# Optimization experiments

Hardware: AMD Instinct MI355X
Metric: run time of the kernel (lower is better)

The kernel has to match this reference:

```python
import jax, jax.numpy as jnp
import numpy as np

B, S, D = 4, 1024, 1024
H, DK = 16, 64
E, DFF, TOPK = 8, 2048, 2
EPS = 1e-5

def setup_inputs() -> dict:
    key = jax.random.key(0)
    ks = jax.random.split(key, 8)
    sd = 0.02
    return {
        "x": jax.random.normal(ks[0], (B, S, D), jnp.float32),
        "Wqkv": jax.random.normal(ks[1], (3 * D, D), jnp.float32) * sd,
        "Wo": jax.random.normal(ks[2], (D, D), jnp.float32) * sd,
        "ln1_g": jnp.ones((D,), jnp.float32),
        "ln1_b": jnp.zeros((D,), jnp.float32),
        "ln2_g": jnp.ones((D,), jnp.float32),
        "ln2_b": jnp.zeros((D,), jnp.float32),
        "Wg": jax.random.normal(ks[3], (E, D), jnp.float32) * sd,
        "W1": jax.random.normal(ks[4], (E, DFF, D), jnp.float32) * sd,
        "W2": jax.random.normal(ks[5], (E, D, DFF), jnp.float32) * sd,
        "res_scale": jnp.ones((1,), jnp.float32),
    }

def _layernorm(x, g, b):
    mu = jnp.mean(x, axis=-1, keepdims=True)
    var = jnp.var(x, axis=-1, keepdims=True)
    return (x - mu) * jax.lax.rsqrt(var + EPS) * g + b

def _mha(x, Wqkv, Wo):
    # fused qkv projection (self-attention branch of original)
    qkv = jnp.einsum('bsd,ed->bse', x, Wqkv)  # [B,S,3D]
    q, k, v = jnp.split(qkv, 3, axis=-1)
    def heads(t):
        return t.reshape(B, S, H, DK).transpose(0, 2, 1, 3)  # [B,H,S,DK]
    q, k, v = heads(q), heads(k), heads(v)
    scores = jnp.einsum('bhqd,bhkd->bhqk', q, k) * (1.0 / np.sqrt(DK))
    attn = jax.nn.softmax(scores, axis=-1)
    ctx = jnp.einsum('bhqk,bhkd->bhqd', attn, v)
    ctx = ctx.transpose(0, 2, 1, 3).reshape(B, S, D)
    return jnp.einsum('bsd,od->bso', ctx, Wo)

def _moe(x, Wg, W1, W2):
    T = B * S
    flat = x.reshape(T, D)
    logits = flat @ Wg.T                      # [T,E]
    probs = jax.nn.softmax(logits, axis=-1)
    rw, sel = jax.lax.top_k(probs, TOPK)      # [T,K]
    rw = rw / jnp.sum(rw, axis=-1, keepdims=True)
    # dense all-experts FFN (faithful to original parallel_apply over all experts)
    h = jax.nn.gelu(jnp.einsum('td,efd->tef', flat, W1), approximate=False)  # [T,E,DFF]
    eo = jnp.einsum('tef,edf->ted', h, W2)    # [T,E,D]
    ew = jnp.zeros((T, E), flat.dtype).at[jnp.arange(T)[:, None], sel].add(rw)
    out = jnp.einsum('te,ted->td', ew, eo).reshape(B, S, D)
    logp = jnp.log(jnp.clip(probs, 1e-6))
    entropy_loss = jnp.mean(-jnp.sum(probs * logp, axis=-1))
    return out, logits, entropy_loss

def reference(x, Wqkv, Wo, ln1_g, ln1_b, ln2_g, ln2_b, Wg, W1, W2, res_scale):
    nx = _layernorm(x, ln1_g, ln1_b)
    x = x + _mha(nx, Wqkv, Wo) * res_scale
    nx = _layernorm(x, ln2_g, ln2_b)
    moe_out, router_logits, entropy_loss = _moe(nx, Wg, W1, W2)
    x = x + moe_out * res_scale
    return x, router_logits, entropy_loss
```

## Files before the change

### kernel.cpp

```cpp
#include <hip/hip_runtime.h>
#include <math.h>


typedef _Float16 f16;
typedef _Float16 f16x8 __attribute__((ext_vector_type(8)));
typedef _Float16 f16x4 __attribute__((ext_vector_type(4)));
typedef float f32x4 __attribute__((ext_vector_type(4)));

#define LO_SCALE 2048.0f
#define INV_LO   (1.0f/2048.0f)
#define INV_W    (1.0f/256.0f)
#define INV_WLO  (1.0f/(256.0f*2048.0f))

#define MFMA16(a, b, c) __builtin_amdgcn_mfma_f32_16x16x32_f16(a, b, c, 0, 0, 0)

__device__ __forceinline__ void gl_lds16(const void* g, void* l) {
  __builtin_amdgcn_global_load_lds(
      (const __attribute__((address_space(1))) void*)g,
      (__attribute__((address_space(3))) void*)l, 16, 0, 0);
}

__global__ __launch_bounds__(256) void cvt_w_kernel(
    const float* __restrict__ in, f16* __restrict__ oh, f16* __restrict__ ol, int n4) {
  const int i = blockIdx.x * 256 + threadIdx.x;
  if (i >= n4) return;
  const float4 v = ((const float4*)in)[i];
  f16x4 hv, lv;
  float a;
  a = v.x * 256.0f; hv[0] = (f16)a; lv[0] = (f16)((a - (float)hv[0]) * LO_SCALE);
  a = v.y * 256.0f; hv[1] = (f16)a; lv[1] = (f16)((a - (float)hv[1]) * LO_SCALE);
  a = v.z * 256.0f; hv[2] = (f16)a; lv[2] = (f16)((a - (float)hv[2]) * LO_SCALE);
  a = v.w * 256.0f; hv[3] = (f16)a; lv[3] = (f16)((a - (float)hv[3]) * LO_SCALE);
  ((f16x4*)oh)[i] = hv;
  ((f16x4*)ol)[i] = lv;
}

__global__ __launch_bounds__(256) void cvt_h_kernel(
    const float* __restrict__ in, f16* __restrict__ out, int n4) {
  const int i = blockIdx.x * 256 + threadIdx.x;
  if (i >= n4) return;
  const float4 v = ((const float4*)in)[i];
  f16x4 ov = {(f16)v.x, (f16)v.y, (f16)v.z, (f16)v.w};
  ((f16x4*)out)[i] = ov;
}

__global__ __launch_bounds__(256) void ln_kernel(
    const float* __restrict__ x, const float* __restrict__ g, const float* __restrict__ bb,
    f16* __restrict__ oh, f16* __restrict__ ol,
    f16* __restrict__ o1,
    float* __restrict__ of)
{
  const int t = blockIdx.x, tid = threadIdx.x;
  const float4 v = ((const float4*)(x + (long)t * 1024))[tid];
  float s  = v.x + v.y + v.z + v.w;
  float sq = v.x*v.x + v.y*v.y + v.z*v.z + v.w*v.w;
#pragma unroll
  for (int m = 1; m < 64; m <<= 1) { s += __shfl_xor(s, m); sq += __shfl_xor(sq, m); }
  __shared__ float red[8];
  const int w = tid >> 6;
  if ((tid & 63) == 0) { red[w] = s; red[4 + w] = sq; }
  __syncthreads();
  s  = red[0] + red[1] + red[2] + red[3];
  sq = red[4] + red[5] + red[6] + red[7];
  const float mu   = s * (1.0f/1024.0f);
  const float var  = sq * (1.0f/1024.0f) - mu*mu;
  const float rstd = 1.0f / sqrtf(var + 1e-5f);
  const float4 gv = ((const float4*)g)[tid];
  const float4 bv = ((const float4*)bb)[tid];
  float o4[4];
  o4[0] = (v.x - mu)*rstd*gv.x + bv.x;
  o4[1] = (v.y - mu)*rstd*gv.y + bv.y;
  o4[2] = (v.z - mu)*rstd*gv.z + bv.z;
  o4[3] = (v.w - mu)*rstd*gv.w + bv.w;
  const long base = (long)t * 1024 + tid * 4;
  if (oh) {
    f16x4 hv, lv;
#pragma unroll
    for (int i = 0; i < 4; ++i) {
      hv[i] = (f16)o4[i];
      lv[i] = (f16)((o4[i] - (float)hv[i]) * LO_SCALE);
    }
    *(f16x4*)(oh + base) = hv;
    *(f16x4*)(ol + base) = lv;
  }
  if (o1) {
    f16x4 ov = {(f16)o4[0], (f16)o4[1], (f16)o4[2], (f16)o4[3]};
    *(f16x4*)(o1 + base) = ov;
  }
  if (of) *(float4*)(of + base) = make_float4(o4[0], o4[1], o4[2], o4[3]);
}

#define GM_QKV 0
#define GM_WO  1

template<int MODE>
__global__ __launch_bounds__(256, 2) void gemm_split_kernel(
    const f16* __restrict__ Ah, const f16* __restrict__ Al,
    const f16* __restrict__ Bh, const f16* __restrict__ Bl,
    f16* __restrict__ Ch, f16* __restrict__ Cl,
    float* __restrict__ Cf,
    const float* __restrict__ xres, const float* __restrict__ rsp,
    int N, int K)
{
  __shared__ __align__(16) f16 sAh[128*32], sAl[128*32], sBh[128*32], sBl[128*32];
  const int tid = threadIdx.x;
  const int l = tid & 63, w = tid >> 6;
  const int wm = w >> 1, wn = w & 1;
  const int tm0 = blockIdx.y * 128, tn0 = blockIdx.x * 128;
  const int kg = l >> 4, r16 = l & 15;
  const int srow = w * 32 + (l >> 2);
  const int scol = (l & 3) * 8;
  const int ldsbase = w * 1024;

  f32x4 am[4][4] = {};
  f32x4 ac[4][4] = {};

  for (int k0 = 0; k0 < K; k0 += 32) {
#pragma unroll
    for (int i = 0; i < 2; ++i) {
      const int row = srow + i * 16;
      const long aoff = (long)(tm0 + row) * K + k0 + scol;
      const long boff = (long)(tn0 + row) * K + k0 + scol;
      const int lo = ldsbase + i * 512;
      gl_lds16(Ah + aoff, &sAh[lo]);
      gl_lds16(Al + aoff, &sAl[lo]);
      gl_lds16(Bh + boff, &sBh[lo]);
      gl_lds16(Bl + boff, &sBl[lo]);
    }
    __syncthreads();
    f16x8 ah[4], al[4], bh[4], bl[4];
#pragma unroll
    for (int m = 0; m < 4; ++m) {
      const int ro = (wm*64 + m*16 + r16) * 32 + kg*8;
      ah[m] = *(const f16x8*)&sAh[ro];
      al[m] = *(const f16x8*)&sAl[ro];
    }
#pragma unroll
    for (int n = 0; n < 4; ++n) {
      const int ro = (wn*64 + n*16 + r16) * 32 + kg*8;
      bh[n] = *(const f16x8*)&sBh[ro];
      bl[n] = *(const f16x8*)&sBl[ro];
    }
#pragma unroll
    for (int m = 0; m < 4; ++m)
#pragma unroll
      for (int n = 0; n < 4; ++n) {
        am[m][n] = MFMA16(ah[m], bh[n], am[m][n]);
        ac[m][n] = MFMA16(ah[m], bl[n], ac[m][n]);
        ac[m][n] = MFMA16(al[m], bh[n], ac[m][n]);
      }
    __syncthreads();
  }

  const float rs = (MODE == GM_WO) ? rsp[0] : 0.0f;
#pragma unroll
  for (int m = 0; m < 4; ++m)
#pragma unroll
    for (int n = 0; n < 4; ++n)
#pragma unroll
      for (int r = 0; r < 4; ++r) {
        const int row = tm0 + wm*64 + m*16 + kg*4 + r;
        const int col = tn0 + wn*64 + n*16 + r16;
        const long idx = (long)row * N + col;
        const float v = am[m][n][r] * INV_W + ac[m][n][r] * INV_WLO;
        if (MODE == GM_QKV) {
          const f16 vh = (f16)v;
          Ch[idx] = vh;
          Cl[idx] = (f16)((v - (float)vh) * LO_SCALE);
        } else {
          Cf[idx] = xres[idx] + rs * v;
        }
      }
}

__global__ __launch_bounds__(256, 2) void attn_kernel(
    const f16* __restrict__ qkh, const f16* __restrict__ qkl,
    f16* __restrict__ ctxh, f16* __restrict__ ctxl)
{
  __shared__ __align__(16) f16 sKh[64*64], sKl[64*64], sVh[64*64], sVl[64*64];
  __shared__ __align__(16) f16 sPh[4*16*64], sPl[4*16*64];
  const int qt = blockIdx.x;
  const int bh = blockIdx.y;
  const int b = bh >> 4, h = bh & 15;
  const int tid = threadIdx.x;
  const int l = tid & 63, w = tid >> 6;
  const int kg = l >> 4, r16 = l & 15;

  const long qbase = (long)(b*1024 + qt*64 + w*16 + r16) * 3072 + h * 64;
  f16x8 aqh[2], aql[2];
#pragma unroll
  for (int c = 0; c < 2; ++c) {
    aqh[c] = *(const f16x8*)(qkh + qbase + c*32 + kg*8);
    aql[c] = *(const f16x8*)(qkl + qbase + c*32 + kg*8);
  }

  f32x4 om[4] = {}; f32x4 oc[4] = {};
  float mrun[4] = {-INFINITY, -INFINITY, -INFINITY, -INFINITY};
  float lrun[4] = {0.f, 0.f, 0.f, 0.f};

  for (int kv0 = 0; kv0 < 1024; kv0 += 64) {
#pragma unroll
    for (int cc = 0; cc < 2; ++cc) {
      const int c = tid + cc * 256;
      const int row = c >> 3, c8 = c & 7;
      const long gb = (long)(b*1024 + kv0 + row) * 3072 + 1024 + h*64 + c8*8;
      const int slot = row*8 + (c8 ^ (row & 7));
      *(uint4*)&sKh[slot*8] = *(const uint4*)(qkh + gb);
      *(uint4*)&sKl[slot*8] = *(const uint4*)(qkl + gb);
      f16 vh8[8], vl8[8];
      *(uint4*)vh8 = *(const uint4*)(qkh + gb + 1024);
      *(uint4*)vl8 = *(const uint4*)(qkl + gb + 1024);
#pragma unroll
      for (int e2 = 0; e2 < 8; ++e2) {
        const int d = c8*8 + e2;
        const int ci = d*64 + (row ^ ((d & 7) << 3));
        sVh[ci] = vh8[e2];
        sVl[ci] = vl8[e2];
      }
    }
    __syncthreads();

    f32x4 sm[4] = {}; f32x4 sc[4] = {};
#pragma unroll
    for (int n = 0; n < 4; ++n) {
      const int krow = n*16 + r16;
#pragma unroll
      for (int c = 0; c < 2; ++c) {
        const int slot = krow*8 + ((c*4 + kg) ^ (krow & 7));
        const f16x8 kh = *(const f16x8*)&sKh[slot*8];
        const f16x8 kl = *(const f16x8*)&sKl[slot*8];
        sm[n] = MFMA16(aqh[c], kh, sm[n]);
        sc[n] = MFMA16(aqh[c], kl, sc[n]);
        sc[n] = MFMA16(aql[c], kh, sc[n]);
      }
    }
    float sval[4][4];
#pragma unroll
    for (int n = 0; n < 4; ++n)
#pragma unroll
      for (int r = 0; r < 4; ++r)
        sval[n][r] = (sm[n][r] + sc[n][r] * INV_LO) * 0.125f;

    float pv[4][4];
#pragma unroll
    for (int r = 0; r < 4; ++r) {
      float mx = fmaxf(fmaxf(sval[0][r], sval[1][r]), fmaxf(sval[2][r], sval[3][r]));
#pragma unroll
      for (int msk = 1; msk < 16; msk <<= 1) mx = fmaxf(mx, __shfl_xor(mx, msk));
      const float mnew = fmaxf(mrun[r], mx);
      const float fsc = expf(mrun[r] - mnew);
      mrun[r] = mnew;
      lrun[r] *= fsc;
#pragma unroll
      for (int n = 0; n < 4; ++n) { om[n][r] *= fsc; oc[n][r] *= fsc; }
      float ps = 0.f;
#pragma unroll
      for (int n = 0; n < 4; ++n) {
        const float p = expf(sval[n][r] - mnew);
        pv[n][r] = p;
        ps += p;
      }
#pragma unroll
      for (int msk = 1; msk < 16; msk <<= 1) ps += __shfl_xor(ps, msk);
      lrun[r] += ps;
    }

#pragma unroll
    for (int n = 0; n < 4; ++n)
#pragma unroll
      for (int r = 0; r < 4; ++r) {
        const int qr = kg*4 + r;
        const int kvc = n*16 + r16;
        const int idx = w*1024 + qr*64 + (kvc ^ ((qr & 7) << 3));
        const float p = pv[n][r];
        const f16 ph = (f16)p;
        sPh[idx] = ph;
        sPl[idx] = (f16)((p - (float)ph) * LO_SCALE);
      }

#pragma unroll
    for (int c = 0; c < 2; ++c) {
      const int pidx = w*1024 + r16*64 + ((c*32 + kg*8) ^ ((r16 & 7) << 3));
      const f16x8 ph = *(const f16x8*)&sPh[pidx];
      const f16x8 pl = *(const f16x8*)&sPl[pidx];
#pragma unroll
      for (int n = 0; n < 4; ++n) {
        const int d = n*16 + r16;
        const int vi = d*64 + ((c*32 + kg*8) ^ ((d & 7) << 3));
        const f16x8 vh = *(const f16x8*)&sVh[vi];
        const f16x8 vl = *(const f16x8*)&sVl[vi];
        om[n] = MFMA16(ph, vh, om[n]);
        oc[n] = MFMA16(ph, vl, oc[n]);
        oc[n] = MFMA16(pl, vh, oc[n]);
      }
    }
    __syncthreads();
  }

  float inv[4];
#pragma unroll
  for (int r = 0; r < 4; ++r) inv[r] = 1.0f / lrun[r];
#pragma unroll
  for (int n = 0; n < 4; ++n)
#pragma unroll
    for (int r = 0; r < 4; ++r) {
      const long t = (long)(b*1024 + qt*64 + w*16 + kg*4 + r);
      const int col = h*64 + n*16 + r16;
      const float val = (om[n][r] + oc[n][r] * INV_LO) * inv[r];
      const f16 vh = (f16)val;
      ctxh[t*1024 + col] = vh;
      ctxl[t*1024 + col] = (f16)((val - (float)vh) * LO_SCALE);
    }
}

__global__ __launch_bounds__(256) void router_kernel(
    const float* __restrict__ nx2f, const float* __restrict__ Wg,
    float* __restrict__ outLogits, float* __restrict__ outEnt,
    int* __restrict__ cnt, int* __restrict__ tok,
    int* __restrict__ pidx, float* __restrict__ pw)
{
  const int tid = threadIdx.x;
  const int l = tid & 63, w = tid >> 6;
  const int t = blockIdx.x * 4 + w;
  const float4* xr = (const float4*)(nx2f + (long)t * 1024);
  float4 xv[4];
#pragma unroll
  for (int i = 0; i < 4; ++i) xv[i] = xr[l*4 + i];
  float lg[8];
#pragma unroll
  for (int e = 0; e < 8; ++e) {
    const float4* wr = (const float4*)(Wg + e * 1024);
    float s = 0.f;
#pragma unroll
    for (int i = 0; i < 4; ++i) {
      const float4 wv = wr[l*4 + i];
      s += xv[i].x*wv.x + xv[i].y*wv.y + xv[i].z*wv.z + xv[i].w*wv.w;
    }
#pragma unroll
    for (int msk = 1; msk < 64; msk <<= 1) s += __shfl_xor(s, msk);
    lg[e] = s;
  }
  float mx = lg[0];
#pragma unroll
  for (int e = 1; e < 8; ++e) mx = fmaxf(mx, lg[e]);
  float den = 0.f, pe[8];
#pragma unroll
  for (int e = 0; e < 8; ++e) { pe[e] = expf(lg[e] - mx); den += pe[e]; }
  const float invd = 1.0f / den;
  float ent = 0.f;
#pragma unroll
  for (int e = 0; e < 8; ++e) {
    const float p = pe[e] * invd;
    ent -= p * logf(fmaxf(p, 1e-6f));
  }
  int s0 = 0; float v0 = lg[0];
#pragma unroll
  for (int e = 1; e < 8; ++e) if (lg[e] > v0) { v0 = lg[e]; s0 = e; }
  int s1 = (s0 == 0) ? 1 : 0; float v1 = -INFINITY;
#pragma unroll
  for (int e = 0; e < 8; ++e) if (e != s0 && lg[e] > v1) { v1 = lg[e]; s1 = e; }
  float w0 = expf(v0 - mx) * invd;
  float w1 = expf(v1 - mx) * invd;
  const float wn = 1.0f / (w0 + w1);
  w0 *= wn; w1 *= wn;

  float myv = lg[0];
#pragma unroll
  for (int e = 1; e < 8; ++e) myv = (l == e) ? lg[e] : myv;
  if (l < 8) outLogits[t*8 + l] = myv;

  if (l == 0) {
    atomicAdd(outEnt, ent * (1.0f / 4096.0f));
    const int sl0 = atomicAdd(&cnt[s0], 1);
    tok[s0*4096 + sl0] = t;
    pidx[t*2 + 0] = s0*4096 + sl0;
    pw[t*2 + 0] = w0;
    const int sl1 = atomicAdd(&cnt[s1], 1);
    tok[s1*4096 + sl1] = t;
    pidx[t*2 + 1] = s1*4096 + sl1;
    pw[t*2 + 1] = w1;
  }
}

__global__ void init_kernel(int* cnt, float* ent) {
  const int i = threadIdx.x;
  if (i < 8) cnt[i] = 0;
  if (i == 8) *ent = 0.f;
}

__global__ void finalize_kernel(const int* __restrict__ cnt, int* __restrict__ offs) {
  if (threadIdx.x == 0) {
    int o = 0;
#pragma unroll
    for (int e = 0; e < 8; ++e) { offs[e] = o; o += cnt[e]; }
  }
}

#define GM_FFN1 0
#define GM_FFN2 1

template<int MODE>
__global__ __launch_bounds__(256, 2) void gemm_moe_kernel(
    const f16* __restrict__ A, const f16* __restrict__ Bw,
    f16* __restrict__ C, int N, int K,
    const int* __restrict__ tok, const int* __restrict__ cnt, const int* __restrict__ offs)
{
  __shared__ __align__(16) f16 sA[128*32], sB[128*32];
  const int e = blockIdx.z;
  const int cntE = cnt[e];
  const int tm0 = blockIdx.y * 128;
  if (tm0 >= cntE) return;
  const int rowOff = offs[e];
  const f16* Bp = Bw + (long)e * N * K;
  const int tid = threadIdx.x;
  const int l = tid & 63, w = tid >> 6;
  const int wm = w >> 1, wn = w & 1;
  const int tn0 = blockIdx.x * 128;
  const int kg = l >> 4, r16 = l & 15;
  const int srow = w*32 + (l >> 2);
  const int scol = (l & 3) * 8;
  const int ldsbase = w * 1024;

  long arow[2];
#pragma unroll
  for (int i = 0; i < 2; ++i) {
    int r = tm0 + srow + i*16;
    if (r > cntE - 1) r = cntE - 1;
    arow[i] = (MODE == GM_FFN1) ? (long)tok[e*4096 + r] : (long)(rowOff + r);
  }

  f32x4 acc[4][4] = {};
  for (int k0 = 0; k0 < K; k0 += 32) {
#pragma unroll
    for (int i = 0; i < 2; ++i) {
      const int row = srow + i*16;
      const int lo = ldsbase + i*512;
      gl_lds16(A + arow[i]*K + k0 + scol, &sA[lo]);
      gl_lds16(Bp + (long)(tn0 + row)*K + k0 + scol, &sB[lo]);
    }
    __syncthreads();
    f16x8 af[4], bfr[4];
#pragma unroll
    for (int m = 0; m < 4; ++m)
      af[m] = *(const f16x8*)&sA[(wm*64 + m*16 + r16)*32 + kg*8];
#pragma unroll
    for (int n = 0; n < 4; ++n)
      bfr[n] = *(const f16x8*)&sB[(wn*64 + n*16 + r16)*32 + kg*8];
#pragma unroll
    for (int m = 0; m < 4; ++m)
#pragma unroll
      for (int n = 0; n < 4; ++n)
        acc[m][n] = MFMA16(af[m], bfr[n], acc[m][n]);
    __syncthreads();
  }

#pragma unroll
  for (int m = 0; m < 4; ++m)
#pragma unroll
    for (int n = 0; n < 4; ++n)
#pragma unroll
      for (int r = 0; r < 4; ++r) {
        const int rr = tm0 + wm*64 + m*16 + kg*4 + r;
        if (rr < cntE) {
          const int col = tn0 + wn*64 + n*16 + r16;
          float v = acc[m][n][r];
          if (MODE == GM_FFN1) v = 0.5f * v * (1.0f + erff(v * 0.70710678118654752f));
          C[(long)(rowOff + rr) * N + col] = (f16)v;
        }
      }
}

__global__ __launch_bounds__(256) void combine_kernel(
    const float* __restrict__ x2, const f16* __restrict__ eo,
    const int* __restrict__ pidx, const float* __restrict__ pw,
    const int* __restrict__ offs, const float* __restrict__ rsp,
    float* __restrict__ out)
{
  const int t = blockIdx.x;
  const int tid = threadIdx.x;
  const int i0 = pidx[t*2], i1 = pidx[t*2 + 1];
  const float w0 = pw[t*2], w1 = pw[t*2 + 1];
  const long r0 = (long)offs[i0 >> 12] + (i0 & 4095);
  const long r1 = (long)offs[i1 >> 12] + (i1 & 4095);
  const float rs = rsp[0];
  const float4 xv = ((const float4*)(x2 + (long)t*1024))[tid];
  const f16x4 e0 = *(const f16x4*)(eo + r0*1024 + tid*4);
  const f16x4 e1 = *(const f16x4*)(eo + r1*1024 + tid*4);
  float4 o;
  o.x = xv.x + rs * (w0*(float)e0[0] + w1*(float)e1[0]);
  o.y = xv.y + rs * (w0*(float)e0[1] + w1*(float)e1[1]);
  o.z = xv.z + rs * (w0*(float)e0[2] + w1*(float)e1[2]);
  o.w = xv.w + rs * (w0*(float)e0[3] + w1*(float)e1[3]);
  ((float4*)(out + (long)t*1024))[tid] = o;
}

extern "C" void kernel_launch(void* const* d_in, const int* in_sizes, int n_in,
                              void* d_out, int out_size, void* d_ws, size_t ws_size,
                              hipStream_t stream)
{
  const float* x    = (const float*)d_in[0];
  const float* Wqkv = (const float*)d_in[1];
  const float* Wo   = (const float*)d_in[2];
  const float* ln1g = (const float*)d_in[3];
  const float* ln1b = (const float*)d_in[4];
  const float* ln2g = (const float*)d_in[5];
  const float* ln2b = (const float*)d_in[6];
  const float* Wg   = (const float*)d_in[7];
  const float* W1   = (const float*)d_in[8];
  const float* W2   = (const float*)d_in[9];
  const float* rsp  = (const float*)d_in[10];
  float* out = (float*)d_out;

  char* p = (char*)d_ws;
  auto alloc = [&](size_t n) { char* r = p; p += (n + 255) & ~(size_t)255; return r; };
  f16*   wqh  = (f16*)alloc(3072L*1024*2);
  f16*   wql  = (f16*)alloc(3072L*1024*2);
  f16*   woh  = (f16*)alloc(1024L*1024*2);
  f16*   wol  = (f16*)alloc(1024L*1024*2);
  f16*   w1h  = (f16*)alloc(8L*2048*1024*2);
  f16*   w2h  = (f16*)alloc(8L*1024*2048*2);
  f16*   nxh  = (f16*)alloc(4096L*1024*2);
  f16*   nxl  = (f16*)alloc(4096L*1024*2);
  f16*   qkh  = (f16*)alloc(4096L*3072*2);
  f16*   qkl  = (f16*)alloc(4096L*3072*2);
  f16*   ctxh = (f16*)alloc(4096L*1024*2);
  f16*   ctxl = (f16*)alloc(4096L*1024*2);
  float* x2   = (float*)alloc(4096L*1024*4);
  f16*   nx2h = (f16*)alloc(4096L*1024*2);
  float* nx2f = (float*)alloc(4096L*1024*4);
  int*   cnt  = (int*)alloc(256);
  int*   offs = (int*)alloc(256);
  int*   tok  = (int*)alloc(8L*4096*4);
  int*   pidx = (int*)alloc(4096L*2*4);
  float* pw   = (float*)alloc(4096L*2*4);
  if ((size_t)(p - (char*)d_ws) > ws_size) return;
  f16* hbuf = qkh;
  f16* eob  = nxh;

  cvt_w_kernel<<<3072*1024/4/256, 256, 0, stream>>>(Wqkv, wqh, wql, 3072*1024/4);
  cvt_w_kernel<<<1024*1024/4/256, 256, 0, stream>>>(Wo, woh, wol, 1024*1024/4);
  cvt_h_kernel<<<8*2048*1024/4/256, 256, 0, stream>>>(W1, w1h, 8*2048*1024/4);
  cvt_h_kernel<<<8*1024*2048/4/256, 256, 0, stream>>>(W2, w2h, 8*1024*2048/4);
  ln_kernel<<<4096, 256, 0, stream>>>(x, ln1g, ln1b, nxh, nxl, nullptr, nullptr);
  gemm_split_kernel<GM_QKV><<<dim3(24, 32), 256, 0, stream>>>(
      nxh, nxl, wqh, wql, qkh, qkl, nullptr, nullptr, nullptr, 3072, 1024);
  attn_kernel<<<dim3(16, 64), 256, 0, stream>>>(qkh, qkl, ctxh, ctxl);
  gemm_split_kernel<GM_WO><<<dim3(8, 32), 256, 0, stream>>>(
      ctxh, ctxl, woh, wol, nullptr, nullptr, x2, x, rsp, 1024, 1024);
  ln_kernel<<<4096, 256, 0, stream>>>(x2, ln2g, ln2b, nullptr, nullptr, nx2h, nx2f);
  init_kernel<<<1, 64, 0, stream>>>(cnt, out + 4227072);
  router_kernel<<<1024, 256, 0, stream>>>(nx2f, Wg, out + 4194304, out + 4227072,
                                          cnt, tok, pidx, pw);
  finalize_kernel<<<1, 64, 0, stream>>>(cnt, offs);
  gemm_moe_kernel<GM_FFN1><<<dim3(16, 32, 8), 256, 0, stream>>>(
      nx2h, w1h, hbuf, 2048, 1024, tok, cnt, offs);
  gemm_moe_kernel<GM_FFN2><<<dim3(8, 32, 8), 256, 0, stream>>>(
      hbuf, w2h, eob, 1024, 2048, tok, cnt, offs);
  combine_kernel<<<4096, 256, 0, stream>>>(x2, eob, pidx, pw, offs, rsp, out);
}
```

Baseline: 787.7 us.

## Pre-transpose V and restructure attention to keep P in registers

Adds a separate kernel that writes V transposed per head, so the attention kernel can stream K and V tiles straight into LDS with async global-to-LDS loads instead of doing a scalar scatter transpose every iteration. The attention kernel swaps MFMA operand order so each lane holds one query column, which makes softmax row reductions two shuffles. P is repacked between lanes with shuffles rather than staged through LDS. Output goes through an LDS transpose for coalesced 16-byte stores. The cost is an extra kernel launch and an extra pass over V in global memory. The transposed V buffer reuses the nx2f workspace, which the second layernorm only writes after attention has finished.

```diff
diff --git a/kernel.cpp b/kernel.cpp
--- a/kernel.cpp
+++ b/kernel.cpp
@@ -18,6 +18,10 @@
   __builtin_amdgcn_global_load_lds(
       (const __attribute__((address_space(1))) void*)g,
       (__attribute__((address_space(3))) void*)l, 16, 0, 0);
+}
+
+__device__ __forceinline__ unsigned int pk2(f16 a, f16 b) {
+  union { f16 h[2]; unsigned int u; } x; x.h[0] = a; x.h[1] = b; return x.u;
 }
 
 __global__ __launch_bounds__(256) void cvt_w_kernel(
@@ -47,8 +51,7 @@
 __global__ __launch_bounds__(256) void ln_kernel(
     const float* __restrict__ x, const float* __restrict__ g, const float* __restrict__ bb,
     f16* __restrict__ oh, f16* __restrict__ ol,
-    f16* __restrict__ o1,
-    float* __restrict__ of)
+    f16* __restrict__ o1, float* __restrict__ of)
 {
   const int t = blockIdx.x, tid = threadIdx.x;
   const float4 v = ((const float4*)(x + (long)t * 1024))[tid];
@@ -173,144 +176,231 @@
       }
 }
 
+__global__ __launch_bounds__(256) void vt_kernel(
+    const f16* __restrict__ qkh, const f16* __restrict__ qkl,
+    f16* __restrict__ vTh, f16* __restrict__ vTl)
+{
+  __shared__ __align__(16) f16 sH[64*72], sL[64*72];
+  const int bh = blockIdx.x, tt = blockIdx.y;
+  const int b = bh >> 4, h = bh & 15;
+  const int t0 = tt * 64;
+  const int tid = threadIdx.x;
+#pragma unroll
+  for (int cc = 0; cc < 2; ++cc) {
+    const int c = tid + cc*256;
+    const int row = c >> 3, p = c & 7;
+    const int pos = p ^ (row & 7) ^ (row >> 3);
+    const long src = (long)(b*1024 + t0 + row)*3072 + 2048 + h*64 + p*8;
+    *(uint4*)&sH[row*72 + pos*8] = *(const uint4*)(qkh + src);
+    *(uint4*)&sL[row*72 + pos*8] = *(const uint4*)(qkl + src);
+  }
+  __syncthreads();
+#pragma unroll
+  for (int cc = 0; cc < 2; ++cc) {
+    const int c = tid + cc*256;
+    const int d = c >> 3, k8 = c & 7;
+    union { f16 h[8]; uint4 u; } oh, ol;
+#pragma unroll
+    for (int e = 0; e < 8; ++e) {
+      const int k = k8*8 + e;
+      const int pos = (d >> 3) ^ (k & 7) ^ (k >> 3);
+      oh.h[e] = sH[k*72 + pos*8 + (d & 7)];
+      ol.h[e] = sL[k*72 + pos*8 + (d & 7)];
+    }
+    const long dst = ((long)bh*64 + d)*1024 + t0 + k8*8;
+    *(uint4*)(vTh + dst) = oh.u;
+    *(uint4*)(vTl + dst) = ol.u;
+  }
+}
+
 __global__ __launch_bounds__(256, 2) void attn_kernel(
     const f16* __restrict__ qkh, const f16* __restrict__ qkl,
+    const f16* __restrict__ vTh, const f16* __restrict__ vTl,
     f16* __restrict__ ctxh, f16* __restrict__ ctxl)
 {
-  __shared__ __align__(16) f16 sKh[64*64], sKl[64*64], sVh[64*64], sVl[64*64];
-  __shared__ __align__(16) f16 sPh[4*16*64], sPl[4*16*64];
-  const int qt = blockIdx.x;
-  const int bh = blockIdx.y;
+  __shared__ __align__(16) f16 smem[16384];
+  f16* sKh = smem;
+  f16* sKl = smem + 4096;
+  f16* sVh = smem + 8192;
+  f16* sVl = smem + 12288;
+
+  const int bh = blockIdx.x, qt = blockIdx.y;
   const int b = bh >> 4, h = bh & 15;
   const int tid = threadIdx.x;
   const int l = tid & 63, w = tid >> 6;
   const int kg = l >> 4, r16 = l & 15;
-
-  const long qbase = (long)(b*1024 + qt*64 + w*16 + r16) * 3072 + h * 64;
-  f16x8 aqh[2], aql[2];
-#pragma unroll
-  for (int c = 0; c < 2; ++c) {
-    aqh[c] = *(const f16x8*)(qkh + qbase + c*32 + kg*8);
-    aql[c] = *(const f16x8*)(qkl + qbase + c*32 + kg*8);
-  }
-
-  f32x4 om[4] = {}; f32x4 oc[4] = {};
-  float mrun[4] = {-INFINITY, -INFINITY, -INFINITY, -INFINITY};
-  float lrun[4] = {0.f, 0.f, 0.f, 0.f};
+  const int ls0 = ((l & 16) << 1) + r16;
+  const int ls1 = ls0 + 16;
+  const bool hi = (l & 32) != 0;
+
+  {
+#pragma unroll
+    for (int cc = 0; cc < 2; ++cc) {
+      const int c = tid + cc*256;
+      const int row = c >> 3, p = c & 7;
+      const int sp = p ^ (row & 7);
+      const long src = (long)(b*1024 + qt*64 + row)*3072 + h*64 + sp*8;
+      gl_lds16(qkh + src, &sKh[c*8]);
+      gl_lds16(qkl + src, &sKl[c*8]);
+    }
+    __syncthreads();
+  }
+  f16x8 bqh[2], bql[2];
+  {
+    const int qrow = w*16 + r16;
+#pragma unroll
+    for (int c = 0; c < 2; ++c) {
+      const int off = qrow*64 + (((c*4 + kg) ^ (qrow & 7))) * 8;
+      bqh[c] = *(const f16x8*)&sKh[off];
+      bql[c] = *(const f16x8*)&sKl[off];
+    }
+    __syncthreads();
+  }
+
+  f32x4 om[4] = {}, oc[4] = {};
+  float mrun = -INFINITY, lrun = 0.f;
 
   for (int kv0 = 0; kv0 < 1024; kv0 += 64) {
 #pragma unroll
     for (int cc = 0; cc < 2; ++cc) {
-      const int c = tid + cc * 256;
-      const int row = c >> 3, c8 = c & 7;
-      const long gb = (long)(b*1024 + kv0 + row) * 3072 + 1024 + h*64 + c8*8;
-      const int slot = row*8 + (c8 ^ (row & 7));
-      *(uint4*)&sKh[slot*8] = *(const uint4*)(qkh + gb);
-      *(uint4*)&sKl[slot*8] = *(const uint4*)(qkl + gb);
-      f16 vh8[8], vl8[8];
-      *(uint4*)vh8 = *(const uint4*)(qkh + gb + 1024);
-      *(uint4*)vl8 = *(const uint4*)(qkl + gb + 1024);
-#pragma unroll
-      for (int e2 = 0; e2 < 8; ++e2) {
-        const int d = c8*8 + e2;
-        const int ci = d*64 + (row ^ ((d & 7) << 3));
-        sVh[ci] = vh8[e2];
-        sVl[ci] = vl8[e2];
-      }
-    }
-    __syncthreads();
-
-    f32x4 sm[4] = {}; f32x4 sc[4] = {};
+      const int c = tid + cc*256;
+      const int row = c >> 3, p = c & 7;
+      const int sp = p ^ (row & 7);
+      const long ksrc = (long)(b*1024 + kv0 + row)*3072 + 1024 + h*64 + sp*8;
+      gl_lds16(qkh + ksrc, &sKh[c*8]);
+      gl_lds16(qkl + ksrc, &sKl[c*8]);
+      const long vsrc = ((long)bh*64 + row)*1024 + kv0 + sp*8;
+      gl_lds16(vTh + vsrc, &sVh[c*8]);
+      gl_lds16(vTl + vsrc, &sVl[c*8]);
+    }
+    __syncthreads();
+
+    f32x4 sm[4] = {}, sc[4] = {};
 #pragma unroll
     for (int n = 0; n < 4; ++n) {
       const int krow = n*16 + r16;
 #pragma unroll
       for (int c = 0; c < 2; ++c) {
-        const int slot = krow*8 + ((c*4 + kg) ^ (krow & 7));
-        const f16x8 kh = *(const f16x8*)&sKh[slot*8];
-        const f16x8 kl = *(const f16x8*)&sKl[slot*8];
-        sm[n] = MFMA16(aqh[c], kh, sm[n]);
-        sc[n] = MFMA16(aqh[c], kl, sc[n]);
-        sc[n] = MFMA16(aql[c], kh, sc[n]);
-      }
-    }
-    float sval[4][4];
+        const int ko = krow*64 + (((c*4 + kg) ^ (krow & 7))) * 8;
+        const f16x8 kh = *(const f16x8*)&sKh[ko];
+        const f16x8 kl = *(const f16x8*)&sKl[ko];
+        sm[n] = MFMA16(kh, bqh[c], sm[n]);
+        sc[n] = MFMA16(kh, bql[c], sc[n]);
+        sc[n] = MFMA16(kl, bqh[c], sc[n]);
+      }
+    }
+
+    float sv[4][4];
+    float mx = -INFINITY;
 #pragma unroll
     for (int n = 0; n < 4; ++n)
 #pragma unroll
-      for (int r = 0; r < 4; ++r)
-        sval[n][r] = (sm[n][r] + sc[n][r] * INV_LO) * 0.125f;
-
-    float pv[4][4];
+      for (int r = 0; r < 4; ++r) {
+        sv[n][r] = (sm[n][r] + sc[n][r] * INV_LO) * 0.125f;
+        mx = fmaxf(mx, sv[n][r]);
+      }
+    mx = fmaxf(mx, __shfl_xor(mx, 16));
+    mx = fmaxf(mx, __shfl_xor(mx, 32));
+    const float mnew = fmaxf(mrun, mx);
+    const float fsc = __expf(mrun - mnew);
+    mrun = mnew;
+    lrun *= fsc;
+#pragma unroll
+    for (int n = 0; n < 4; ++n) { om[n] *= fsc; oc[n] *= fsc; }
+    float pp[4][4];
+    float ps = 0.f;
+#pragma unroll
+    for (int n = 0; n < 4; ++n)
+#pragma unroll
+      for (int r = 0; r < 4; ++r) {
+        pp[n][r] = __expf(sv[n][r] - mnew);
+        ps += pp[n][r];
+      }
+    ps += __shfl_xor(ps, 16);
+    ps += __shfl_xor(ps, 32);
+    lrun += ps;
+
+    unsigned int wh_[4][2], wl_[4][2];
+#pragma unroll
+    for (int n = 0; n < 4; ++n)
+#pragma unroll
+      for (int hh = 0; hh < 2; ++hh) {
+        const float p0 = pp[n][2*hh], p1 = pp[n][2*hh+1];
+        const f16 h0 = (f16)p0, h1 = (f16)p1;
+        wh_[n][hh] = pk2(h0, h1);
+        wl_[n][hh] = pk2((f16)((p0 - (float)h0) * LO_SCALE),
+                         (f16)((p1 - (float)h1) * LO_SCALE));
+      }
+
+#pragma unroll
+    for (int c = 0; c < 2; ++c) {
+      union { unsigned int u[4]; f16x8 v; } pah, pal;
+      {
+        const unsigned int* A = wh_[2*c];
+        const unsigned int* B = wh_[2*c+1];
+        unsigned int t0 = __shfl((int)A[0], ls0), u0 = __shfl((int)B[0], ls0);
+        unsigned int t1 = __shfl((int)A[1], ls0), u1 = __shfl((int)B[1], ls0);
+        unsigned int t2 = __shfl((int)A[0], ls1), u2 = __shfl((int)B[0], ls1);
+        unsigned int t3 = __shfl((int)A[1], ls1), u3 = __shfl((int)B[1], ls1);
+        pah.u[0] = hi ? u0 : t0; pah.u[1] = hi ? u1 : t1;
+        pah.u[2] = hi ? u2 : t2; pah.u[3] = hi ? u3 : t3;
+      }
+      {
+        const unsigned int* A = wl_[2*c];
+        const unsigned int* B = wl_[2*c+1];
+        unsigned int t0 = __shfl((int)A[0], ls0), u0 = __shfl((int)B[0], ls0);
+        unsigned int t1 = __shfl((int)A[1], ls0), u1 = __shfl((int)B[1], ls0);
+        unsigned int t2 = __shfl((int)A[0], ls1), u2 = __shfl((int)B[0], ls1);
+        unsigned int t3 = __shfl((int)A[1], ls1), u3 = __shfl((int)B[1], ls1);
+        pal.u[0] = hi ? u0 : t0; pal.u[1] = hi ? u1 : t1;
+        pal.u[2] = hi ? u2 : t2; pal.u[3] = hi ? u3 : t3;
+      }
+#pragma unroll
+      for (int n = 0; n < 4; ++n) {
+        const int vrow = n*16 + r16;
+        const int vo = vrow*64 + (((c*4 + kg) ^ (vrow & 7))) * 8;
+        const f16x8 vh = *(const f16x8*)&sVh[vo];
+        const f16x8 vl = *(const f16x8*)&sVl[vo];
+        om[n] = MFMA16(vh, pah.v, om[n]);
+        oc[n] = MFMA16(vh, pal.v, oc[n]);
+        oc[n] = MFMA16(vl, pah.v, oc[n]);
+      }
+    }
+    __syncthreads();
+  }
+
+  const float inv = 1.0f / lrun;
+  f16 oh16[4][4], ol16[4][4];
+#pragma unroll
+  for (int n = 0; n < 4; ++n)
 #pragma unroll
     for (int r = 0; r < 4; ++r) {
-      float mx = fmaxf(fmaxf(sval[0][r], sval[1][r]), fmaxf(sval[2][r], sval[3][r]));
-#pragma unroll
-      for (int msk = 1; msk < 16; msk <<= 1) mx = fmaxf(mx, __shfl_xor(mx, msk));
-      const float mnew = fmaxf(mrun[r], mx);
-      const float fsc = expf(mrun[r] - mnew);
-      mrun[r] = mnew;
-      lrun[r] *= fsc;
-#pragma unroll
-      for (int n = 0; n < 4; ++n) { om[n][r] *= fsc; oc[n][r] *= fsc; }
-      float ps = 0.f;
-#pragma unroll
-      for (int n = 0; n < 4; ++n) {
-        const float p = expf(sval[n][r] - mnew);
-        pv[n][r] = p;
-        ps += p;
-      }
-#pragma unroll
-      for (int msk = 1; msk < 16; msk <<= 1) ps += __shfl_xor(ps, msk);
-      lrun[r] += ps;
-    }
-
-#pragma unroll
-    for (int n = 0; n < 4; ++n)
-#pragma unroll
-      for (int r = 0; r < 4; ++r) {
-        const int qr = kg*4 + r;
-        const int kvc = n*16 + r16;
-        const int idx = w*1024 + qr*64 + (kvc ^ ((qr & 7) << 3));
-        const float p = pv[n][r];
-        const f16 ph = (f16)p;
-        sPh[idx] = ph;
-        sPl[idx] = (f16)((p - (float)ph) * LO_SCALE);
-      }
-
-#pragma unroll
-    for (int c = 0; c < 2; ++c) {
-      const int pidx = w*1024 + r16*64 + ((c*32 + kg*8) ^ ((r16 & 7) << 3));
-      const f16x8 ph = *(const f16x8*)&sPh[pidx];
-      const f16x8 pl = *(const f16x8*)&sPl[pidx];
-#pragma unroll
-      for (int n = 0; n < 4; ++n) {
-        const int d = n*16 + r16;
-        const int vi = d*64 + ((c*32 + kg*8) ^ ((d & 7) << 3));
-        const f16x8 vh = *(const f16x8*)&sVh[vi];
-        const f16x8 vl = *(const f16x8*)&sVl[vi];
-        om[n] = MFMA16(ph, vh, om[n]);
-        oc[n] = MFMA16(ph, vl, oc[n]);
-        oc[n] = MFMA16(pl, vh, oc[n]);
-      }
-    }
-    __syncthreads();
-  }
-
-  float inv[4];
-#pragma unroll
-  for (int r = 0; r < 4; ++r) inv[r] = 1.0f / lrun[r];
-#pragma unroll
-  for (int n = 0; n < 4; ++n)
-#pragma unroll
-    for (int r = 0; r < 4; ++r) {
-      const long t = (long)(b*1024 + qt*64 + w*16 + kg*4 + r);
-      const int col = h*64 + n*16 + r16;
-      const float val = (om[n][r] + oc[n][r] * INV_LO) * inv[r];
-      const f16 vh = (f16)val;
-      ctxh[t*1024 + col] = vh;
-      ctxl[t*1024 + col] = (f16)((val - (float)vh) * LO_SCALE);
-    }
+      const float v = (om[n][r] + oc[n][r] * INV_LO) * inv;
+      oh16[n][r] = (f16)v;
+      ol16[n][r] = (f16)((v - (float)oh16[n][r]) * LO_SCALE);
+    }
+  f16* sT = smem;
+  const int qloc = w*16 + r16;
+#pragma unroll
+  for (int pass = 0; pass < 2; ++pass) {
+#pragma unroll
+    for (int n = 0; n < 4; ++n) {
+      f16x4 v4;
+#pragma unroll
+      for (int r = 0; r < 4; ++r) v4[r] = pass ? ol16[n][r] : oh16[n][r];
+      *(f16x4*)&sT[qloc*72 + n*16 + kg*4] = v4;
+    }
+    __syncthreads();
+    f16* dst = pass ? ctxl : ctxh;
+#pragma unroll
+    for (int cc = 0; cc < 2; ++cc) {
+      const int c = tid + cc*256;
+      const int q = c >> 3, dc = c & 7;
+      const uint4 vv = *(const uint4*)&sT[q*72 + dc*8];
+      *(uint4*)(dst + (long)(b*1024 + qt*64 + q)*1024 + h*64 + dc*8) = vv;
+    }
+    __syncthreads();
+  }
 }
 
 __global__ __launch_bounds__(256) void router_kernel(
@@ -536,6 +626,8 @@
   if ((size_t)(p - (char*)d_ws) > ws_size) return;
   f16* hbuf = qkh;
   f16* eob  = nxh;
+  f16* vTh  = (f16*)nx2f;
+  f16* vTl  = vTh + 4096L*1024;
 
   cvt_w_kernel<<<3072*1024/4/256, 256, 0, stream>>>(Wqkv, wqh, wql, 3072*1024/4);
   cvt_w_kernel<<<1024*1024/4/256, 256, 0, stream>>>(Wo, woh, wol, 1024*1024/4);
@@ -544,7 +636,8 @@
   ln_kernel<<<4096, 256, 0, stream>>>(x, ln1g, ln1b, nxh, nxl, nullptr, nullptr);
   gemm_split_kernel<GM_QKV><<<dim3(24, 32), 256, 0, stream>>>(
       nxh, nxl, wqh, wql, qkh, qkl, nullptr, nullptr, nullptr, 3072, 1024);
-  attn_kernel<<<dim3(16, 64), 256, 0, stream>>>(qkh, qkl, ctxh, ctxl);
+  vt_kernel<<<dim3(64, 16), 256, 0, stream>>>(qkh, qkl, vTh, vTl);
+  attn_kernel<<<dim3(64, 16), 256, 0, stream>>>(qkh, qkl, vTh, vTl, ctxh, ctxl);
   gemm_split_kernel<GM_WO><<<dim3(8, 32), 256, 0, stream>>>(
       ctxh, ctxl, woh, wol, nullptr, nullptr, x2, x, rsp, 1024, 1024);
   ln_kernel<<<4096, 256, 0, stream>>>(x2, ln2g, ln2b, nullptr, nullptr, nx2h, nx2f);
```

After: 734.7 us. 6.7% less time.
